# Optimization experiments

Hardware: AMD Instinct MI355X
Metric: run time of the kernel (lower is better)

The kernel has to match this reference:

```python
import jax, jax.numpy as jnp
import numpy as np

N = 50000   # nodes
E = 400000  # edges per relation
R = 3       # relations
IN, HID, OUT, H = 256, 64, 64, 4
NEG_SLOPE = 0.2


def setup_inputs() -> dict:
    key = jax.random.key(0)
    ks = jax.random.split(key, 16)
    w = lambda k, shape, s: jax.random.normal(k, shape, jnp.float32) * s
    sW = 1.0 / np.sqrt(IN)  # ~xavier scale (all fan-ins are 256)
    return {
        "x":   w(ks[0], (N, IN), 1.0),
        "src": jax.random.randint(ks[1], (R, E), 0, N, jnp.int32),
        "dst": jax.random.randint(ks[2], (R, E), 0, N, jnp.int32),
        "W0":  w(ks[3], (R, IN, H * HID), sW),
        "al0": w(ks[4], (R, H, HID), 0.1),
        "ar0": w(ks[5], (R, H, HID), 0.1),
        "b0":  jnp.zeros((R, H * HID), jnp.float32),
        "W1":  w(ks[6], (R, H * HID, H * HID), sW),
        "al1": w(ks[7], (R, H, HID), 0.1),
        "ar1": w(ks[8], (R, H, HID), 0.1),
        "b1":  jnp.zeros((R, H * HID), jnp.float32),
        "W2":  w(ks[9], (R, H * HID, H * OUT), sW),
        "al2": w(ks[10], (R, H, OUT), 0.1),
        "ar2": w(ks[11], (R, H, OUT), 0.1),
        "b2":  jnp.zeros((R, H * OUT), jnp.float32),
    }


def gat_conv(h, src, dst, W, al, ar, b):
    """One DGL-style GATConv with elu activation. h: (N, F_in)."""
    heads, d = al.shape
    feat = (h @ W).reshape(-1, heads, d)               # (N, H, D)
    el = jnp.einsum('nhd,hd->nh', feat, al)            # (N, H)
    er = jnp.einsum('nhd,hd->nh', feat, ar)
    e = jax.nn.leaky_relu(el[src] + er[dst], NEG_SLOPE)  # (E, H)
    # segment softmax over incoming edges of each dst node
    emax = jax.ops.segment_max(e, dst, num_segments=N)
    ex = jnp.exp(e - emax[dst])
    denom = jax.ops.segment_sum(ex, dst, num_segments=N)
    alpha = ex / jnp.maximum(denom[dst], 1e-9)         # (E, H)
    msg = feat[src] * alpha[:, :, None]                # (E, H, D)
    out = jax.ops.segment_sum(msg, dst, num_segments=N)  # (N, H, D)
    out = out + b.reshape(heads, d)
    return jax.nn.elu(out)


def _rgat(x, src, dst, params):
    h = x
    for li, (W, al, ar, b) in enumerate(params):
        outs = [gat_conv(h, src[r], dst[r], W[r], al[r], ar[r], b[r]) for r in range(R)]
        o = sum(outs) / R                              # cross-relation mean, (N, H, D)
        h = o.mean(1) if li == 2 else o.reshape(N, -1)
    return h


def reference(x, src, dst, W0, al0, ar0, b0, W1, al1, ar1, b1, W2, al2, ar2, b2):
    params = [(W0, al0, ar0, b0), (W1, al1, ar1, b1), (W2, al2, ar2, b2)]
    return _rgat(x, src, dst, params)
```

## Files before the change

kernel.cpp:

```cpp
#include <hip/hip_runtime.h>
#include <hip/hip_bf16.h>

#define N_NODES 50000
#define N_EDGES 400000
#define N_REL   3
#define NEG_SLOPE 0.2f
#define RP_STRIDE 50016
#define SCAN_BLOCKS 49
#define M_TILES 391
#define MG_PER_XCD 49
#define M_PAD 50048
#define MAXDEG 48

typedef __bf16 bf16x8 __attribute__((ext_vector_type(8)));
typedef float  f32x4  __attribute__((ext_vector_type(4)));

static __device__ __forceinline__ float bf2f(unsigned short u) {
  return __uint_as_float(((unsigned)u) << 16);
}
static __device__ __forceinline__ unsigned short f2bf(float f) {
  union { float f; unsigned u; } x; x.f = f;
  unsigned r = x.u + 0x7FFFu + ((x.u >> 16) & 1u);
  return (unsigned short)(r >> 16);
}
static __device__ __forceinline__ void gld16(const void* g, unsigned short* lds) {
  __builtin_amdgcn_global_load_lds(
      (const __attribute__((address_space(1))) unsigned int*)g,
      (__attribute__((address_space(3))) unsigned int*)lds, 16, 0, 0);
}


__global__ void count_kernel(const int* __restrict__ dst, int* __restrict__ cnt, int total) {
  int i = blockIdx.x * 256 + threadIdx.x;
  if (i < total) {
    int r = i / N_EDGES;
    atomicAdd(&cnt[r * N_NODES + dst[i]], 1);
  }
}

__global__ void block_reduce_kernel(const int* __restrict__ cnt, int* __restrict__ psum) {
  __shared__ int s[256];
  int r = blockIdx.x / SCAN_BLOCKS, b = blockIdx.x % SCAN_BLOCKS;
  int node = b * 1024 + threadIdx.x * 4;
  int sum = 0;
  if (node + 3 < N_NODES) {
    int4 v = *(const int4*)&cnt[r * N_NODES + node];
    sum = v.x + v.y + v.z + v.w;
  } else {
    for (int j = 0; j < 4; j++)
      if (node + j < N_NODES) sum += cnt[r * N_NODES + node + j];
  }
  s[threadIdx.x] = sum;
  __syncthreads();
  for (int o = 128; o > 0; o >>= 1) {
    if (threadIdx.x < o) s[threadIdx.x] += s[threadIdx.x + o];
    __syncthreads();
  }
  if (threadIdx.x == 0) psum[r * SCAN_BLOCKS + b] = s[0];
}

__global__ void psum_scan_kernel(int* __restrict__ psum, int* __restrict__ row_ptr) {
  int r = blockIdx.x, t = threadIdx.x;
  int v = (t < SCAN_BLOCKS) ? psum[r * SCAN_BLOCKS + t] : 0;
  int incl = v;
#pragma unroll
  for (int o = 1; o < 64; o <<= 1) {
    int u = __shfl_up(incl, o);
    if (t >= o) incl += u;
  }
  if (t < SCAN_BLOCKS) psum[r * SCAN_BLOCKS + t] = incl - v;
  if (t == SCAN_BLOCKS - 1) row_ptr[r * RP_STRIDE + N_NODES] = incl;
}

__global__ void scan_write_kernel(const int* __restrict__ cnt, const int* __restrict__ psum,
                                  int* __restrict__ row_ptr, int* __restrict__ cursor) {
  __shared__ int s[256];
  int r = blockIdx.x / SCAN_BLOCKS, b = blockIdx.x % SCAN_BLOCKS;
  int tid = threadIdx.x;
  int node = b * 1024 + tid * 4;
  int c[4] = {0, 0, 0, 0};
  if (node + 3 < N_NODES) {
    int4 v = *(const int4*)&cnt[r * N_NODES + node];
    c[0] = v.x; c[1] = v.y; c[2] = v.z; c[3] = v.w;
  } else {
    for (int j = 0; j < 4; j++)
      if (node + j < N_NODES) c[j] = cnt[r * N_NODES + node + j];
  }
  int tsum = c[0] + c[1] + c[2] + c[3];
  s[tid] = tsum;
  __syncthreads();
  for (int o = 1; o < 256; o <<= 1) {
    int v = (tid >= o) ? s[tid - o] : 0;
    __syncthreads();
    s[tid] += v;
    __syncthreads();
  }
  int run = s[tid] - tsum + psum[r * SCAN_BLOCKS + b];
  if (node + 3 < N_NODES) {
    int4 rp = make_int4(run, run + c[0], run + c[0] + c[1], run + c[0] + c[1] + c[2]);
    *(int4*)&row_ptr[r * RP_STRIDE + node] = rp;
    *(int4*)&cursor[r * N_NODES + node] = rp;
  } else {
    for (int j = 0; j < 4; j++) {
      if (node + j < N_NODES) {
        row_ptr[r * RP_STRIDE + node + j] = run;
        cursor[r * N_NODES + node + j] = run;
      }
      run += c[j];
    }
  }
}

__global__ void scatter_kernel(const int* __restrict__ src, const int* __restrict__ dst,
                               int* __restrict__ cursor, int* __restrict__ col, int total) {
  int i = blockIdx.x * 256 + threadIdx.x;
  if (i < total) {
    int r = i / N_EDGES;
    int d = dst[i];
    int pos = atomicAdd(&cursor[r * N_NODES + d], 1);
    col[r * N_EDGES + pos] = src[i];
  }
}


__global__ void xsplit_kernel(const float* __restrict__ x, unsigned short* __restrict__ xh) {
  int i = blockIdx.x * 256 + threadIdx.x;
  int row = i >> 6;
  float4 v = make_float4(0.f, 0.f, 0.f, 0.f);
  if (row < N_NODES) v = ((const float4*)x)[i];
  ushort4 h;
  h.x = f2bf(v.x); h.y = f2bf(v.y); h.z = f2bf(v.z); h.w = f2bf(v.w);
  ((ushort4*)xh)[i] = h;
}


__global__ void wsplit_kernel(const float* __restrict__ W0, const float* __restrict__ W1,
                              const float* __restrict__ W2,
                              unsigned short* __restrict__ Whi, unsigned short* __restrict__ Wlo) {
  __shared__ float tile[32][33];
  int mat = blockIdx.x >> 6;
  int t = blockIdx.x & 63;
  int k0 = (t >> 3) * 32, n0 = (t & 7) * 32;
  const float* W = (mat < 3 ? W0 : (mat < 6 ? W1 : W2)) + (size_t)(mat % 3) * 65536;
  int row = threadIdx.x >> 3;
  int c4 = threadIdx.x & 7;
  float4 v = *(const float4*)&W[(k0 + row) * 256 + n0 + c4 * 4];
  tile[c4 * 4 + 0][row] = v.x;
  tile[c4 * 4 + 1][row] = v.y;
  tile[c4 * 4 + 2][row] = v.z;
  tile[c4 * 4 + 3][row] = v.w;
  __syncthreads();
  int nl = threadIdx.x >> 3;
  int kq = threadIdx.x & 7;
  ushort4 h, l;
  float a0 = tile[nl][kq * 4 + 0], a1 = tile[nl][kq * 4 + 1];
  float a2 = tile[nl][kq * 4 + 2], a3 = tile[nl][kq * 4 + 3];
  h.x = f2bf(a0); l.x = f2bf(a0 - bf2f(h.x));
  h.y = f2bf(a1); l.y = f2bf(a1 - bf2f(h.y));
  h.z = f2bf(a2); l.z = f2bf(a2 - bf2f(h.z));
  h.w = f2bf(a3); l.w = f2bf(a3 - bf2f(h.w));
  size_t o = (size_t)mat * 65536 + (n0 + nl) * 256 + k0 + kq * 4;
  *(ushort4*)&Whi[o] = h;
  *(ushort4*)&Wlo[o] = l;
}


#define LDS_S 32
#define LDT  136

__global__ __launch_bounds__(256, 3) void gemm_mfma_kernel(
    const unsigned short* __restrict__ Ah,
    const unsigned short* __restrict__ Bhi, const unsigned short* __restrict__ Blo,
    const float* __restrict__ alf, const float* __restrict__ arf,
    unsigned short* __restrict__ Cb, float* __restrict__ el, float* __restrict__ er, int M) {
  __shared__ __align__(16) unsigned short lds[128 * LDT];
  unsigned short* As_h = lds;
  unsigned short* Bs_h = lds + 128 * LDS_S;
  unsigned short* Bs_l = lds + 2 * 128 * LDS_S;

  const int wid = blockIdx.x;
  const int xcd = wid & 7, local = wid >> 3;
  const int m_t = (local / 6) * 8 + xcd;
  if (m_t >= M_TILES) return;
  const int n_t = local % 6;
  const int m0 = m_t * 128, n0 = n_t * 128;

  const int tid = threadIdx.x;
  const int wave = tid >> 6, lane = tid & 63;
  const int quad = lane >> 4, l16 = lane & 15;
  const int wr = wave & 1, wc = wave >> 1;

  f32x4 acc[4][4];
#pragma unroll
  for (int i = 0; i < 4; i++)
#pragma unroll
    for (int j = 0; j < 4; j++) acc[i][j] = (f32x4){0.f, 0.f, 0.f, 0.f};

  for (int kb = 0; kb < 8; kb++) {
    int k0 = kb * 32;
#pragma unroll
    for (int i = 0; i < 2; i++) {
      int ch = wave * 2 + i;
      int c = ch * 64 + lane;
      int row = c >> 2, k16 = c & 3;
      size_t gA = ((size_t)(m0 + row) * 256 + k0) * 2 + (size_t)k16 * 16;
      size_t gB = ((size_t)(n0 + row) * 256 + k0) * 2 + (size_t)k16 * 16;
      gld16((const char*)Ah + gA, &As_h[ch * 512]);
      gld16((const char*)Bhi + gB, &Bs_h[ch * 512]);
      gld16((const char*)Blo + gB, &Bs_l[ch * 512]);
    }
    __syncthreads();

    bf16x8 ah[4], bh[4], bl[4];
#pragma unroll
    for (int t = 0; t < 4; t++) {
      int arow = (wr * 64 + t * 16 + l16) * LDS_S + quad * 8;
      int brow = (wc * 64 + t * 16 + l16) * LDS_S + quad * 8;
      ah[t] = *(const bf16x8*)&As_h[arow];
      bh[t] = *(const bf16x8*)&Bs_h[brow];
      bl[t] = *(const bf16x8*)&Bs_l[brow];
    }
#pragma unroll
    for (int mi = 0; mi < 4; mi++)
#pragma unroll
      for (int ni = 0; ni < 4; ni++) {
        acc[mi][ni] = __builtin_amdgcn_mfma_f32_16x16x32_bf16(ah[mi], bl[ni], acc[mi][ni], 0, 0, 0);
        acc[mi][ni] = __builtin_amdgcn_mfma_f32_16x16x32_bf16(ah[mi], bh[ni], acc[mi][ni], 0, 0, 0);
      }
    __syncthreads();
  }

  const int hw = n_t * 2 + wc;
  const int rel = hw >> 2, hh = hw & 3;
  float alw[4], arw[4];
#pragma unroll
  for (int ni = 0; ni < 4; ni++) {
    int gc = n0 + wc * 64 + ni * 16 + l16;
    alw[ni] = alf[gc]; arw[ni] = arf[gc];
  }
  float pel[4][4], per_[4][4];
#pragma unroll
  for (int mi = 0; mi < 4; mi++)
#pragma unroll
    for (int r = 0; r < 4; r++) {
      float se = 0.f, sr = 0.f;
#pragma unroll
      for (int ni = 0; ni < 4; ni++) {
        se += acc[mi][ni][r] * alw[ni];
        sr += acc[mi][ni][r] * arw[ni];
      }
      pel[mi][r] = se; per_[mi][r] = sr;
    }
#pragma unroll
  for (int off = 1; off < 16; off <<= 1)
#pragma unroll
    for (int mi = 0; mi < 4; mi++)
#pragma unroll
      for (int r = 0; r < 4; r++) {
        pel[mi][r] += __shfl_xor(pel[mi][r], off);
        per_[mi][r] += __shfl_xor(per_[mi][r], off);
      }
  if (l16 == 0) {
#pragma unroll
    for (int mi = 0; mi < 4; mi++)
#pragma unroll
      for (int r = 0; r < 4; r++) {
        int gm = m0 + wr * 64 + mi * 16 + quad * 4 + r;
        if (gm < M) {
          size_t o = ((size_t)rel * N_NODES + gm) * 4 + hh;
          el[o] = pel[mi][r];
          er[o] = per_[mi][r];
        }
      }
  }

#pragma unroll
  for (int mi = 0; mi < 4; mi++) {
    int row = wr * 64 + mi * 16 + quad * 4;
#pragma unroll
    for (int ni = 0; ni < 4; ni++) {
      int c = wc * 64 + ni * 16 + l16;
#pragma unroll
      for (int r = 0; r < 4; r++)
        lds[(row + r) * LDT + c] = f2bf(acc[mi][ni][r]);
    }
  }
  __syncthreads();
#pragma unroll
  for (int it = 0; it < 8; it++) {
    int chunk = tid + 256 * it;
    int row = chunk >> 4, c8 = (chunk & 15) * 8;
    int gm = m0 + row;
    if (gm < M)
      *(uint4*)&Cb[(size_t)gm * 768 + n0 + c8] = *(const uint4*)&lds[row * LDT + c8];
  }
}


__global__ void agg_kernel(const unsigned short* __restrict__ featb,
                           const float* __restrict__ el, const float* __restrict__ er,
                           const int* __restrict__ row_ptr, const int* __restrict__ col,
                           const float* __restrict__ bias,
                           unsigned short* __restrict__ hH, float* __restrict__ outF,
                           int final_layer) {
  __shared__ float salpha[4][N_REL][MAXDEG * 4];
  int w = threadIdx.x >> 6;
  int n = blockIdx.x * 4 + w;
  int L = threadIdx.x & 63;
  if (n >= N_NODES) return;
  const int hsel = L >> 4;

  int s0r[N_REL], s1r[N_REL];
  float invsel[N_REL];
  float4 ernr[N_REL];
#pragma unroll
  for (int r = 0; r < N_REL; r++) {
    int s0 = row_ptr[r * RP_STRIDE + n], s1 = row_ptr[r * RP_STRIDE + n + 1];
    s0r[r] = s0; s1r[r] = s1;
    int deg = s1 - s0;
    float4 ern = ((const float4*)er)[(size_t)r * N_NODES + n];
    ernr[r] = ern;
    const int* cp = col + (size_t)r * N_EDGES;
    bool fits = (deg <= MAXDEG);
    float d0 = 0.f, d1 = 0.f, d2 = 0.f, d3 = 0.f;
    for (int base = s0; base < s1; base += 64) {
      int i = base + L;
      if (i < s1) {
        int s = cp[i];
        float4 els = ((const float4*)el)[(size_t)r * N_NODES + s];
        float e0 = els.x + ern.x; e0 = e0 > 0.f ? e0 : NEG_SLOPE * e0;
        float e1 = els.y + ern.y; e1 = e1 > 0.f ? e1 : NEG_SLOPE * e1;
        float e2 = els.z + ern.z; e2 = e2 > 0.f ? e2 : NEG_SLOPE * e2;
        float e3 = els.w + ern.w; e3 = e3 > 0.f ? e3 : NEG_SLOPE * e3;
        float p0 = __expf(e0), p1 = __expf(e1), p2 = __expf(e2), p3 = __expf(e3);
        if (fits) *(float4*)&salpha[w][r][(i - s0) * 4] = make_float4(p0, p1, p2, p3);
        d0 += p0; d1 += p1; d2 += p2; d3 += p3;
      }
    }
#pragma unroll
    for (int o = 1; o < 64; o <<= 1) {
      d0 += __shfl_xor(d0, o); d1 += __shfl_xor(d1, o);
      d2 += __shfl_xor(d2, o); d3 += __shfl_xor(d3, o);
    }
    float dsel = (hsel == 0) ? d0 : (hsel == 1) ? d1 : (hsel == 2) ? d2 : d3;
    invsel[r] = 1.0f / fmaxf(dsel, 1e-30f);
  }

  const float third = 1.0f / 3.0f;
  float os0 = 0.f, os1 = 0.f, os2 = 0.f, os3 = 0.f;
#pragma unroll
  for (int r = 0; r < N_REL; r++) {
    int s0 = s0r[r], s1 = s1r[r], deg = s1 - s0;
    const int* cp = col + (size_t)r * N_EDGES;
    const unsigned short* fbase = featb + r * 256 + 4 * L;
    float a0 = 0.f, a1 = 0.f, a2 = 0.f, a3 = 0.f;
    if (deg <= MAXDEG) {
      const float* ap = &salpha[w][r][0];
      int i = 0;
      for (; i + 1 < deg; i += 2) {
        int sA = cp[s0 + i], sB = cp[s0 + i + 1];
        float wA = ap[i * 4 + hsel];
        float wB = ap[(i + 1) * 4 + hsel];
        ushort4 fA = *(const ushort4*)&fbase[(size_t)sA * 768];
        ushort4 fB = *(const ushort4*)&fbase[(size_t)sB * 768];
        a0 += wA * bf2f(fA.x) + wB * bf2f(fB.x);
        a1 += wA * bf2f(fA.y) + wB * bf2f(fB.y);
        a2 += wA * bf2f(fA.z) + wB * bf2f(fB.z);
        a3 += wA * bf2f(fA.w) + wB * bf2f(fB.w);
      }
      if (i < deg) {
        int sA = cp[s0 + i];
        float wA = ap[i * 4 + hsel];
        ushort4 fA = *(const ushort4*)&fbase[(size_t)sA * 768];
        a0 += wA * bf2f(fA.x); a1 += wA * bf2f(fA.y);
        a2 += wA * bf2f(fA.z); a3 += wA * bf2f(fA.w);
      }
    } else {
      float4 ern = ernr[r];
      float ernh = (hsel == 0) ? ern.x : (hsel == 1) ? ern.y : (hsel == 2) ? ern.z : ern.w;
      for (int i = s0; i < s1; i++) {
        int s = cp[i];
        float4 els = ((const float4*)el)[(size_t)r * N_NODES + s];
        float elh = (hsel == 0) ? els.x : (hsel == 1) ? els.y : (hsel == 2) ? els.z : els.w;
        float e = elh + ernh; e = e > 0.f ? e : NEG_SLOPE * e;
        float pw = __expf(e);
        ushort4 fA = *(const ushort4*)&fbase[(size_t)s * 768];
        a0 += pw * bf2f(fA.x); a1 += pw * bf2f(fA.y);
        a2 += pw * bf2f(fA.z); a3 += pw * bf2f(fA.w);
      }
    }
    float inv = invsel[r];
    float4 bv = *(const float4*)&bias[r * 256 + 4 * L];
    float o0 = a0 * inv + bv.x, o1 = a1 * inv + bv.y;
    float o2 = a2 * inv + bv.z, o3 = a3 * inv + bv.w;
    o0 = o0 > 0.f ? o0 : __expf(o0) - 1.0f;
    o1 = o1 > 0.f ? o1 : __expf(o1) - 1.0f;
    o2 = o2 > 0.f ? o2 : __expf(o2) - 1.0f;
    o3 = o3 > 0.f ? o3 : __expf(o3) - 1.0f;
    os0 += o0 * third; os1 += o1 * third; os2 += o2 * third; os3 += o3 * third;
  }
  if (final_layer) {
#pragma unroll
    for (int o = 16; o <= 32; o <<= 1) {
      os0 += __shfl_xor(os0, o); os1 += __shfl_xor(os1, o);
      os2 += __shfl_xor(os2, o); os3 += __shfl_xor(os3, o);
    }
    if (L < 16)
      *(float4*)&outF[(size_t)n * 64 + L * 4] =
          make_float4(0.25f * os0, 0.25f * os1, 0.25f * os2, 0.25f * os3);
  } else {
    ushort4 h;
    h.x = f2bf(os0); h.y = f2bf(os1); h.z = f2bf(os2); h.w = f2bf(os3);
    *(ushort4*)&hH[(size_t)n * 256 + 4 * L] = h;
  }
}


extern "C" void kernel_launch(void* const* d_in, const int* in_sizes, int n_in,
                              void* d_out, int out_size, void* d_ws, size_t ws_size,
                              hipStream_t stream) {
  (void)in_sizes; (void)n_in; (void)out_size; (void)ws_size;
  const float* x = (const float*)d_in[0];
  const int* src = (const int*)d_in[1];
  const int* dst = (const int*)d_in[2];
  const float* Wl[3]  = {(const float*)d_in[3], (const float*)d_in[7], (const float*)d_in[11]};
  const float* alL[3] = {(const float*)d_in[4], (const float*)d_in[8], (const float*)d_in[12]};
  const float* arL[3] = {(const float*)d_in[5], (const float*)d_in[9], (const float*)d_in[13]};
  const float* bL[3]  = {(const float*)d_in[6], (const float*)d_in[10], (const float*)d_in[14]};

  char* p = (char*)d_ws;
  auto alloc = [&](size_t bytes) {
    char* q = p;
    p += (bytes + 255) & ~size_t(255);
    return q;
  };
  unsigned short* xh = (unsigned short*)alloc((size_t)M_PAD * 256 * 2);
  unsigned short* hH = (unsigned short*)alloc((size_t)M_PAD * 256 * 2);
  unsigned short* featb = (unsigned short*)alloc((size_t)N_NODES * 768 * 2);
  float* el      = (float*)alloc((size_t)N_REL * N_NODES * 4 * 4);
  float* er      = (float*)alloc((size_t)N_REL * N_NODES * 4 * 4);
  int*   cnt     = (int*)alloc((size_t)N_REL * N_NODES * 4);
  int*   cursor  = (int*)alloc((size_t)N_REL * N_NODES * 4);
  int*   row_ptr = (int*)alloc((size_t)N_REL * RP_STRIDE * 4 + 64);
  int*   col     = (int*)alloc((size_t)N_REL * N_EDGES * 4);
  int*   psum    = (int*)alloc((size_t)N_REL * SCAN_BLOCKS * 4);
  unsigned short* Whi = (unsigned short*)alloc((size_t)9 * 65536 * 2);
  unsigned short* Wlo = (unsigned short*)alloc((size_t)9 * 65536 * 2);

  hipMemsetAsync(cnt, 0, (size_t)N_REL * N_NODES * 4, stream);
  const int totalE = N_REL * N_EDGES;
  count_kernel<<<(totalE + 255) / 256, 256, 0, stream>>>(dst, cnt, totalE);
  block_reduce_kernel<<<N_REL * SCAN_BLOCKS, 256, 0, stream>>>(cnt, psum);
  psum_scan_kernel<<<N_REL, 64, 0, stream>>>(psum, row_ptr);
  scan_write_kernel<<<N_REL * SCAN_BLOCKS, 256, 0, stream>>>(cnt, psum, row_ptr, cursor);
  scatter_kernel<<<(totalE + 255) / 256, 256, 0, stream>>>(src, dst, cursor, col, totalE);
  wsplit_kernel<<<9 * 64, 256, 0, stream>>>(Wl[0], Wl[1], Wl[2], Whi, Wlo);
  xsplit_kernel<<<M_PAD * 64 / 256, 256, 0, stream>>>(x, xh);

  const int nodeBlocks = (N_NODES + 3) / 4;
  const int gemmBlocks = MG_PER_XCD * 6 * 8;
  for (int l = 0; l < 3; l++) {
    const unsigned short* Ahp = (l == 0) ? xh : hH;
    gemm_mfma_kernel<<<gemmBlocks, 256, 0, stream>>>(
        Ahp, Whi + (size_t)l * 3 * 65536, Wlo + (size_t)l * 3 * 65536,
        alL[l], arL[l], featb, el, er, N_NODES);
    agg_kernel<<<nodeBlocks, 256, 0, stream>>>(
        featb, el, er, row_ptr, col, bL[l], hH, (float*)d_out, l == 2);
  }
}
```

Baseline: 851.6 us.

## Restructure GAT aggregation: batched edge loads, LDS index cache, 8-way gather unroll

The aggregation kernel now issues the column-index and el loads for all three relations up front, so their latencies overlap instead of running one after another. It stores the pre-normalized alpha and the source indices in LDS for low-degree nodes. The gather loop is unrolled 8 and 4 wide, using readfirstlane scalar addresses, so more feature loads are in flight at once. This costs extra LDS and registers, which may lower occupancy, and the high-degree path keeps the old per-edge loop.

```diff
diff --git a/kernel.cpp b/kernel.cpp
--- a/kernel.cpp
+++ b/kernel.cpp
@@ -304,6 +304,7 @@
                            unsigned short* __restrict__ hH, float* __restrict__ outF,
                            int final_layer) {
   __shared__ float salpha[4][N_REL][MAXDEG * 4];
+  __shared__ int   sidx[4][N_REL][MAXDEG];
   int w = threadIdx.x >> 6;
   int n = blockIdx.x * 4 + w;
   int L = threadIdx.x & 63;
@@ -313,28 +314,53 @@
   int s0r[N_REL], s1r[N_REL];
   float invsel[N_REL];
   float4 ernr[N_REL];
+
+  int sv[N_REL];
+  bool val[N_REL], fastp[N_REL];
 #pragma unroll
   for (int r = 0; r < N_REL; r++) {
     int s0 = row_ptr[r * RP_STRIDE + n], s1 = row_ptr[r * RP_STRIDE + n + 1];
     s0r[r] = s0; s1r[r] = s1;
     int deg = s1 - s0;
-    float4 ern = ((const float4*)er)[(size_t)r * N_NODES + n];
-    ernr[r] = ern;
-    const int* cp = col + (size_t)r * N_EDGES;
-    bool fits = (deg <= MAXDEG);
-    float d0 = 0.f, d1 = 0.f, d2 = 0.f, d3 = 0.f;
-    for (int base = s0; base < s1; base += 64) {
-      int i = base + L;
-      if (i < s1) {
-        int s = cp[i];
-        float4 els = ((const float4*)el)[(size_t)r * N_NODES + s];
-        float e0 = els.x + ern.x; e0 = e0 > 0.f ? e0 : NEG_SLOPE * e0;
-        float e1 = els.y + ern.y; e1 = e1 > 0.f ? e1 : NEG_SLOPE * e1;
-        float e2 = els.z + ern.z; e2 = e2 > 0.f ? e2 : NEG_SLOPE * e2;
-        float e3 = els.w + ern.w; e3 = e3 > 0.f ? e3 : NEG_SLOPE * e3;
-        float p0 = __expf(e0), p1 = __expf(e1), p2 = __expf(e2), p3 = __expf(e3);
-        if (fits) *(float4*)&salpha[w][r][(i - s0) * 4] = make_float4(p0, p1, p2, p3);
-        d0 += p0; d1 += p1; d2 += p2; d3 += p3;
+    fastp[r] = (deg <= 64);
+    int i = s0 + L;
+    val[r] = fastp[r] && (i < s1);
+    sv[r] = 0;
+    if (val[r]) sv[r] = col[(size_t)r * N_EDGES + i];
+    ernr[r] = ((const float4*)er)[(size_t)r * N_NODES + n];
+  }
+  float4 ev[N_REL];
+#pragma unroll
+  for (int r = 0; r < N_REL; r++) {
+    ev[r] = make_float4(0.f, 0.f, 0.f, 0.f);
+    if (val[r]) ev[r] = ((const float4*)el)[(size_t)r * N_NODES + sv[r]];
+  }
+#pragma unroll
+  for (int r = 0; r < N_REL; r++) {
+    float4 ern = ernr[r];
+    float p0 = 0.f, p1 = 0.f, p2 = 0.f, p3 = 0.f;
+    if (val[r]) {
+      float e0 = ev[r].x + ern.x; e0 = e0 > 0.f ? e0 : NEG_SLOPE * e0;
+      float e1 = ev[r].y + ern.y; e1 = e1 > 0.f ? e1 : NEG_SLOPE * e1;
+      float e2 = ev[r].z + ern.z; e2 = e2 > 0.f ? e2 : NEG_SLOPE * e2;
+      float e3 = ev[r].w + ern.w; e3 = e3 > 0.f ? e3 : NEG_SLOPE * e3;
+      p0 = __expf(e0); p1 = __expf(e1); p2 = __expf(e2); p3 = __expf(e3);
+    }
+    float d0 = p0, d1 = p1, d2 = p2, d3 = p3;
+    if (!fastp[r]) {
+      int s0 = s0r[r], s1 = s1r[r];
+      const int* cp = col + (size_t)r * N_EDGES;
+      for (int base = s0; base < s1; base += 64) {
+        int i = base + L;
+        if (i < s1) {
+          int s = cp[i];
+          float4 els = ((const float4*)el)[(size_t)r * N_NODES + s];
+          float e0 = els.x + ern.x; e0 = e0 > 0.f ? e0 : NEG_SLOPE * e0;
+          float e1 = els.y + ern.y; e1 = e1 > 0.f ? e1 : NEG_SLOPE * e1;
+          float e2 = els.z + ern.z; e2 = e2 > 0.f ? e2 : NEG_SLOPE * e2;
+          float e3 = els.w + ern.w; e3 = e3 > 0.f ? e3 : NEG_SLOPE * e3;
+          d0 += __expf(e0); d1 += __expf(e1); d2 += __expf(e2); d3 += __expf(e3);
+        }
       }
     }
 #pragma unroll
@@ -342,62 +368,109 @@
       d0 += __shfl_xor(d0, o); d1 += __shfl_xor(d1, o);
       d2 += __shfl_xor(d2, o); d3 += __shfl_xor(d3, o);
     }
-    float dsel = (hsel == 0) ? d0 : (hsel == 1) ? d1 : (hsel == 2) ? d2 : d3;
-    invsel[r] = 1.0f / fmaxf(dsel, 1e-30f);
+    float i0 = 1.0f / fmaxf(d0, 1e-30f), i1 = 1.0f / fmaxf(d1, 1e-30f);
+    float i2 = 1.0f / fmaxf(d2, 1e-30f), i3 = 1.0f / fmaxf(d3, 1e-30f);
+    invsel[r] = (hsel == 0) ? i0 : (hsel == 1) ? i1 : (hsel == 2) ? i2 : i3;
+    int deg = s1r[r] - s0r[r];
+    if (val[r] && deg <= MAXDEG) {
+      *(float4*)&salpha[w][r][L * 4] = make_float4(p0 * i0, p1 * i1, p2 * i2, p3 * i3);
+      sidx[w][r][L] = sv[r];
+    }
   }
 
   const float third = 1.0f / 3.0f;
+  const int roffL = 4 * L;
   float os0 = 0.f, os1 = 0.f, os2 = 0.f, os3 = 0.f;
 #pragma unroll
   for (int r = 0; r < N_REL; r++) {
     int s0 = s0r[r], s1 = s1r[r], deg = s1 - s0;
-    const int* cp = col + (size_t)r * N_EDGES;
-    const unsigned short* fbase = featb + r * 256 + 4 * L;
+    const int roff = r * 256 + roffL;
     float a0 = 0.f, a1 = 0.f, a2 = 0.f, a3 = 0.f;
     if (deg <= MAXDEG) {
       const float* ap = &salpha[w][r][0];
+      const int* ip = &sidx[w][r][0];
       int i = 0;
-      for (; i + 1 < deg; i += 2) {
-        int sA = cp[s0 + i], sB = cp[s0 + i + 1];
+      for (; i + 8 <= deg; i += 8) {
+        int s_[8];
+#pragma unroll
+        for (int j = 0; j < 8; j++) s_[j] = ip[i + j];
+        ushort4 f_[8];
+#pragma unroll
+        for (int j = 0; j < 8; j++) {
+          size_t ro = (size_t)(unsigned)__builtin_amdgcn_readfirstlane(s_[j]) * 768;
+          f_[j] = *(const ushort4*)&featb[ro + roff];
+        }
+        float w_[8];
+#pragma unroll
+        for (int j = 0; j < 8; j++) w_[j] = ap[(i + j) * 4 + hsel];
+#pragma unroll
+        for (int j = 0; j < 8; j++) {
+          a0 += w_[j] * bf2f(f_[j].x);
+          a1 += w_[j] * bf2f(f_[j].y);
+          a2 += w_[j] * bf2f(f_[j].z);
+          a3 += w_[j] * bf2f(f_[j].w);
+        }
+      }
+      for (; i + 4 <= deg; i += 4) {
+        int s_[4];
+#pragma unroll
+        for (int j = 0; j < 4; j++) s_[j] = ip[i + j];
+        ushort4 f_[4];
+#pragma unroll
+        for (int j = 0; j < 4; j++) {
+          size_t ro = (size_t)(unsigned)__builtin_amdgcn_readfirstlane(s_[j]) * 768;
+          f_[j] = *(const ushort4*)&featb[ro + roff];
+        }
+        float w_[4];
+#pragma unroll
+        for (int j = 0; j < 4; j++) w_[j] = ap[(i + j) * 4 + hsel];
+#pragma unroll
+        for (int j = 0; j < 4; j++) {
+          a0 += w_[j] * bf2f(f_[j].x);
+          a1 += w_[j] * bf2f(f_[j].y);
+          a2 += w_[j] * bf2f(f_[j].z);
+          a3 += w_[j] * bf2f(f_[j].w);
+        }
+      }
+      for (; i < deg; i++) {
+        int sA = ip[i];
+        size_t ro = (size_t)(unsigned)__builtin_amdgcn_readfirstlane(sA) * 768;
+        ushort4 fA = *(const ushort4*)&featb[ro + roff];
         float wA = ap[i * 4 + hsel];
-        float wB = ap[(i + 1) * 4 + hsel];
-        ushort4 fA = *(const ushort4*)&fbase[(size_t)sA * 768];
-        ushort4 fB = *(const ushort4*)&fbase[(size_t)sB * 768];
-        a0 += wA * bf2f(fA.x) + wB * bf2f(fB.x);
-        a1 += wA * bf2f(fA.y) + wB * bf2f(fB.y);
-        a2 += wA * bf2f(fA.z) + wB * bf2f(fB.z);
-        a3 += wA * bf2f(fA.w) + wB * bf2f(fB.w);
-      }
-      if (i < deg) {
-        int sA = cp[s0 + i];
-        float wA = ap[i * 4 + hsel];
-        ushort4 fA = *(const ushort4*)&fbase[(size_t)sA * 768];
         a0 += wA * bf2f(fA.x); a1 += wA * bf2f(fA.y);
         a2 += wA * bf2f(fA.z); a3 += wA * bf2f(fA.w);
       }
+      float4 bv = *(const float4*)&bias[r * 256 + roffL];
+      float o0 = a0 + bv.x, o1 = a1 + bv.y, o2 = a2 + bv.z, o3 = a3 + bv.w;
+      o0 = o0 > 0.f ? o0 : __expf(o0) - 1.0f;
+      o1 = o1 > 0.f ? o1 : __expf(o1) - 1.0f;
+      o2 = o2 > 0.f ? o2 : __expf(o2) - 1.0f;
+      o3 = o3 > 0.f ? o3 : __expf(o3) - 1.0f;
+      os0 += o0 * third; os1 += o1 * third; os2 += o2 * third; os3 += o3 * third;
     } else {
       float4 ern = ernr[r];
       float ernh = (hsel == 0) ? ern.x : (hsel == 1) ? ern.y : (hsel == 2) ? ern.z : ern.w;
+      const int* cp = col + (size_t)r * N_EDGES;
       for (int i = s0; i < s1; i++) {
         int s = cp[i];
         float4 els = ((const float4*)el)[(size_t)r * N_NODES + s];
         float elh = (hsel == 0) ? els.x : (hsel == 1) ? els.y : (hsel == 2) ? els.z : els.w;
         float e = elh + ernh; e = e > 0.f ? e : NEG_SLOPE * e;
         float pw = __expf(e);
-        ushort4 fA = *(const ushort4*)&fbase[(size_t)s * 768];
+        ushort4 fA = *(const ushort4*)&featb[(size_t)s * 768 + roff];
         a0 += pw * bf2f(fA.x); a1 += pw * bf2f(fA.y);
         a2 += pw * bf2f(fA.z); a3 += pw * bf2f(fA.w);
       }
-    }
-    float inv = invsel[r];
-    float4 bv = *(const float4*)&bias[r * 256 + 4 * L];
-    float o0 = a0 * inv + bv.x, o1 = a1 * inv + bv.y;
-    float o2 = a2 * inv + bv.z, o3 = a3 * inv + bv.w;
-    o0 = o0 > 0.f ? o0 : __expf(o0) - 1.0f;
-    o1 = o1 > 0.f ? o1 : __expf(o1) - 1.0f;
-    o2 = o2 > 0.f ? o2 : __expf(o2) - 1.0f;
-    o3 = o3 > 0.f ? o3 : __expf(o3) - 1.0f;
-    os0 += o0 * third; os1 += o1 * third; os2 += o2 * third; os3 += o3 * third;
+      float inv = invsel[r];
+      float4 bv = *(const float4*)&bias[r * 256 + roffL];
+      float o0 = a0 * inv + bv.x, o1 = a1 * inv + bv.y;
+      float o2 = a2 * inv + bv.z, o3 = a3 * inv + bv.w;
+      o0 = o0 > 0.f ? o0 : __expf(o0) - 1.0f;
+      o1 = o1 > 0.f ? o1 : __expf(o1) - 1.0f;
+      o2 = o2 > 0.f ? o2 : __expf(o2) - 1.0f;
+      o3 = o3 > 0.f ? o3 : __expf(o3) - 1.0f;
+      os0 += o0 * third; os1 += o1 * third; os2 += o2 * third; os3 += o3 * third;
+    }
   }
   if (final_layer) {
 #pragma unroll
```

Result: faster. 763.4 us (-10.4%).
